# Kernel tuning notes

Measured on AMD Instinct MI355X. Metric: run time of the kernel, lower is better.

The kernel has to match this reference:

```python
import jax, jax.numpy as jnp
import numpy as np

D_LATENTS = 256
B, N = 8, 4096
EPS = 1e-5  # BatchNorm eps (torch default)


def _w(k, shape):
    return jax.random.normal(k, shape, jnp.float32) * 0.05


def setup_inputs() -> dict:
    key = jax.random.key(0)
    ks = jax.random.split(key, 20)
    d4, d2, d = D_LATENTS // 4, D_LATENTS // 2, D_LATENTS
    def bn(k):
        k1, k2 = jax.random.split(k)
        g = 1.0 + 0.1 * jax.random.normal(k1, (0,), jnp.float32)  # placeholder
        return g
    inp = {
        "x": jax.random.normal(ks[0], (B, 3, N), jnp.float32),
        "conv1_w": _w(ks[1], (d4, 3)),
        "bn1_g": 1.0 + 0.1 * jax.random.normal(ks[2], (d4,), jnp.float32),
        "bn1_b": 0.1 * jax.random.normal(ks[3], (d4,), jnp.float32),
        "conv2_w": _w(ks[4], (d4, d4)),
        "bn2_g": 1.0 + 0.1 * jax.random.normal(ks[5], (d4,), jnp.float32),
        "bn2_b": 0.1 * jax.random.normal(ks[6], (d4,), jnp.float32),
        "le0_w1": _w(ks[7], (d2, d2)),
        "le0_g1": 1.0 + 0.1 * jax.random.normal(ks[8], (d2,), jnp.float32),
        "le0_b1": 0.1 * jax.random.normal(ks[9], (d2,), jnp.float32),
        "le0_w2": _w(ks[10], (d2, d2)),
        "le0_g2": 1.0 + 0.1 * jax.random.normal(ks[11], (d2,), jnp.float32),
        "le0_b2": 0.1 * jax.random.normal(ks[12], (d2,), jnp.float32),
        "le1_w1": _w(ks[13], (d, d)),
        "le1_g1": 1.0 + 0.1 * jax.random.normal(ks[14], (d,), jnp.float32),
        "le1_b1": 0.1 * jax.random.normal(ks[15], (d,), jnp.float32),
        "le1_w2": _w(ks[16], (d, d)),
        "le1_g2": 1.0 + 0.1 * jax.random.normal(ks[17], (d,), jnp.float32),
        "le1_b2": 0.1 * jax.random.normal(ks[18], (d,), jnp.float32),
    }
    return inp


def _bn_relu(y, g, b, axes, ch_axis):
    # BatchNorm (training-mode batch stats, biased var like torch) + ReLU
    m = jnp.mean(y, axes, keepdims=True)
    v = jnp.var(y, axes, keepdims=True)
    shp = [1] * y.ndim
    shp[ch_axis] = -1
    return jax.nn.relu((y - m) * jax.lax.rsqrt(v + EPS) * g.reshape(shp) + b.reshape(shp))


def _square_distance(src, dst):
    # src [B,S,3], dst [B,N,3] -> [B,S,N]
    return (jnp.sum(src * src, -1, keepdims=True)
            - 2.0 * jnp.einsum('bsc,bnc->bsn', src, dst)
            + jnp.sum(dst * dst, -1)[:, None, :])


def _fps(xyz, npoint):
    # farthest point sampling, deterministic start at index 0
    Bb, Nn, _ = xyz.shape
    def step(carry, _):
        dist_min, farthest = carry
        centroid = jnp.take_along_axis(xyz, farthest[:, None, None], axis=1)  # [B,1,3]
        d = jnp.sum((xyz - centroid) ** 2, -1)  # [B,N]
        dist_min = jnp.minimum(dist_min, d)
        nxt = jnp.argmax(dist_min, -1).astype(jnp.int32)
        return (dist_min, nxt), farthest
    init = (jnp.full((Bb, Nn), 1e10, xyz.dtype), jnp.zeros((Bb,), jnp.int32))
    _, idxs = jax.lax.scan(step, init, None, length=npoint)
    return jnp.transpose(idxs)  # [B, npoint]


def _sample_and_group(npoint, nsample, xyz, points):
    # PCT-style: FPS centers, kNN neighbors (radius unused), concat(rel, center)
    Bb = xyz.shape[0]
    fps_idx = _fps(xyz, npoint)                       # [B,S]
    bidx = jnp.arange(Bb)[:, None]
    new_xyz = xyz[bidx, fps_idx]                      # [B,S,3]
    new_pts = points[bidx, fps_idx]                   # [B,S,D]
    d2 = _square_distance(new_xyz, xyz)               # [B,S,N]
    _, knn_idx = jax.lax.top_k(-d2, nsample)          # [B,S,ns]
    grouped = points[jnp.arange(Bb)[:, None, None], knn_idx]  # [B,S,ns,D]
    center = new_pts[:, :, None, :]
    feat = jnp.concatenate([grouped - center,
                            jnp.broadcast_to(center, grouped.shape)], axis=-1)
    return new_xyz, feat  # [B,S,3], [B,S,ns,2D]


def _local_encoder(x4, w1, g1, b1, w2, g2, b2):
    # x4: [b,n,s,d] -> conv1x1/bn/relu x2 over channel dim, max over s -> [b,out,n]
    y = jnp.einsum('bnsd,od->bnos', x4, w1)
    y = _bn_relu(y, g1, b1, (0, 1, 3), 2)
    y = jnp.einsum('bnis,oi->bnos', y, w2)
    y = _bn_relu(y, g2, b2, (0, 1, 3), 2)
    y = jnp.max(y, axis=3)                # [b,n,out]
    return jnp.transpose(y, (0, 2, 1))    # [b,out,n]


def reference(x, conv1_w, bn1_g, bn1_b, conv2_w, bn2_g, bn2_b,
              le0_w1, le0_g1, le0_b1, le0_w2, le0_g2, le0_b2,
              le1_w1, le1_g1, le1_b1, le1_w2, le1_g2, le1_b2):
    xyz = jnp.transpose(x, (0, 2, 1))                 # [B,N,3]
    y = jnp.einsum('bcn,oc->bon', x, conv1_w)
    y = _bn_relu(y, bn1_g, bn1_b, (0, 2), 1)
    y = jnp.einsum('bcn,oc->bon', y, conv2_w)
    y = _bn_relu(y, bn2_g, bn2_b, (0, 2), 1)
    pts = jnp.transpose(y, (0, 2, 1))                 # [B,N,d4]
    new_xyz, feat = _sample_and_group(512, 32, xyz, pts)       # [B,512,32,d2]
    f0 = _local_encoder(feat, le0_w1, le0_g1, le0_b1, le0_w2, le0_g2, le0_b2)  # [B,d2,512]
    pts1 = jnp.transpose(f0, (0, 2, 1))
    _, feat2 = _sample_and_group(256, 32, new_xyz, pts1)       # [B,256,32,d]
    f1 = _local_encoder(feat2, le1_w1, le1_g1, le1_b1, le1_w2, le1_g2, le1_b2)  # [B,d,256]
    return f1
```

## Files before the change

### kernel.cpp

```cpp
#include <hip/hip_runtime.h>

constexpr int B_  = 8;
constexpr int N_  = 4096;
constexpr int NP1 = 512;
constexpr int NP2 = 256;
constexpr float EPS_ = 1e-5f;

typedef __attribute__((ext_vector_type(8))) short bhalf8;
typedef __attribute__((ext_vector_type(4))) float f32x4;

__device__ inline short f2bf(float f) {
  union { float fv; unsigned u; } v; v.fv = f;
  unsigned r = v.u + 0x7FFFu + ((v.u >> 16) & 1u);
  return (short)(r >> 16);
}
__device__ inline float bf2f(short s) {
  return __uint_as_float(((unsigned)(unsigned short)s) << 16);
}

template<int CTRL>
__device__ inline void dpp_amax(unsigned &khi, unsigned &klo) {
  unsigned ohi = (unsigned)__builtin_amdgcn_mov_dpp((int)khi, CTRL, 0xF, 0xF, false);
  unsigned olo = (unsigned)__builtin_amdgcn_mov_dpp((int)klo, CTRL, 0xF, 0xF, false);
  if (ohi > khi || (ohi == khi && olo > klo)) { khi = ohi; klo = olo; }
}
__device__ inline void swz16_amax(unsigned &khi, unsigned &klo) {
  unsigned ohi = (unsigned)__builtin_amdgcn_ds_swizzle((int)khi, 0x401F);
  unsigned olo = (unsigned)__builtin_amdgcn_ds_swizzle((int)klo, 0x401F);
  if (ohi > khi || (ohi == khi && olo > klo)) { khi = ohi; klo = olo; }
}
__device__ inline void x32_amax(unsigned &khi, unsigned &klo) {
  unsigned ohi = (unsigned)__shfl_xor((int)khi, 32);
  unsigned olo = (unsigned)__shfl_xor((int)klo, 32);
  if (ohi > khi || (ohi == khi && olo > klo)) { khi = ohi; klo = olo; }
}
__device__ inline unsigned ford(float f) {
  unsigned u = __float_as_uint(f);
  return u ^ (((unsigned)((int)u >> 31)) | 0x80000000u);
}

constexpr int S_BN1 = 0;
constexpr int S_BN2 = 128;
constexpr int S_L0A = 256;
constexpr int S_L0B = 512;
constexpr int S_L1A = 768;
constexpr int S_L1B = 1280;
constexpr int S_TOTAL = 1792;

constexpr size_t OFF_T1   = 0;
constexpr size_t OFF_YBUF = OFF_T1   + 2097152;
constexpr size_t OFF_PTS1 = OFF_YBUF + 16777216;
constexpr size_t OFF_NXYZ = OFF_PTS1 + 524288;
constexpr size_t OFF_WT2C = OFF_NXYZ + 12288;
constexpr size_t OFF_BW0A = OFF_WT2C + 4096;
constexpr size_t OFF_BW0B = OFF_BW0A + 8192;
constexpr size_t OFF_BW1A = OFF_BW0B + 8192;
constexpr size_t OFF_BW1B = OFF_BW1A + 32768;
constexpr size_t OFF_STAT = OFF_BW1B + 32768;
constexpr size_t OFF_CNT  = OFF_STAT + S_TOTAL;
constexpr size_t OFF_INT  = OFF_CNT + 32;

__device__ inline void prep_elem(int idx, const float* __restrict__ conv2w,
                                 const float* __restrict__ w0a, const float* __restrict__ w0b,
                                 const float* __restrict__ w1a, const float* __restrict__ w1b,
                                 float* __restrict__ wt2c,
                                 short* __restrict__ b0a, short* __restrict__ b0b,
                                 short* __restrict__ b1a, short* __restrict__ b1b) {
  if (idx < 4096) { int d = idx >> 6, o = idx & 63; wt2c[idx] = conv2w[o*64 + d]; return; }
  idx -= 4096;
  const float* w; short* dst; int D;
  if      (idx <  2048) { w = w0a; dst = b0a; D = 128; }
  else if (idx <  4096) { w = w0b; dst = b0b; D = 128; idx -= 2048; }
  else if (idx < 12288) { w = w1a; dst = b1a; D = 256; idx -= 4096; }
  else                  { w = w1b; dst = b1b; D = 256; idx -= 12288; }
  int kblk = idx / D, o = idx % D;
  const float* src = w + (size_t)o*D + kblk*8;
  bhalf8 pk;
#pragma unroll
  for (int j = 0; j < 8; ++j) pk[j] = f2bf(src[j]);
  *(bhalf8*)&dst[(size_t)idx*8] = pk;
}

struct FpsSmem {
  float lx[4096], ly[4096], lz[4096];
  float sx[512], sy[512], sz[512];
  unsigned long long wk[2][8];
  int seli1[512];
  int seli2[256];
};
struct ConvSmem {
  float xs[3][64];
  float redS[4][64], redQ[4][64];
  float sc[64], sh[64];
  float at[64*68];
};

__global__ __launch_bounds__(256) void front_kernel(
    const float* __restrict__ x,
    const float* __restrict__ conv1w, const float* __restrict__ bn1g, const float* __restrict__ bn1b,
    const float* __restrict__ conv2w, const float* __restrict__ bn2g, const float* __restrict__ bn2b,
    const float* __restrict__ w0a, const float* __restrict__ w0b,
    const float* __restrict__ w1a, const float* __restrict__ w1b,
    float* __restrict__ wt2c,
    short* __restrict__ b0a, short* __restrict__ b0b,
    short* __restrict__ b1a, short* __restrict__ b1b,
    float* __restrict__ t1, float* __restrict__ t2,
    float* __restrict__ stats, int* __restrict__ cnt,
    int* __restrict__ sel1, float* __restrict__ nxyz, int* __restrict__ sel2) {
  __shared__ __align__(16) char smem_raw[sizeof(FpsSmem)];
  int t = threadIdx.x;
  if (blockIdx.x < 8) {
    constexpr int NPTS = 4096, NSEL1 = 512, NSEL2 = 256, NT = 256;
    constexpr int K = NPTS / NT, NS = NT / 32;
    FpsSmem& S = *reinterpret_cast<FpsSmem*>(smem_raw);
    int b = blockIdx.x;
    int lane = t & 63, wid = t >> 6;
    const float* cb = x + (size_t)b * 3 * NPTS;
    for (int i = t; i < NPTS; i += NT) {
      S.lx[i] = cb[i]; S.ly[i] = cb[NPTS + i]; S.lz[i] = cb[2*NPTS + i];
    }
    __syncthreads();
    float px[K], py[K], pz[K], dm[K];
#pragma unroll
    for (int k = 0; k < K; ++k) {
      int p = t + k*NT;
      px[k] = S.lx[p]; py[k] = S.ly[p]; pz[k] = S.lz[p];
      dm[k] = 1e10f;
    }
    float cx = S.lx[0], cy = S.ly[0], cz = S.lz[0];
    if (t == 0) { S.seli1[0] = 0; S.sx[0] = cx; S.sy[0] = cy; S.sz[0] = cz; }
    for (int it = 1; it < NSEL1; ++it) {
      float bv = -1.f; int bi = 0;
#pragma unroll
      for (int k = 0; k < K; ++k) {
        float dx = px[k]-cx, dy = py[k]-cy, dz = pz[k]-cz;
        float d = dx*dx + dy*dy + dz*dz;
        float nd = fminf(dm[k], d);
        dm[k] = nd;
        if (nd > bv) { bv = nd; bi = t + k*NT; }
      }
      unsigned khi = __float_as_uint(bv), klo = ~(unsigned)bi;
      dpp_amax<0xB1>(khi, klo);
      dpp_amax<0x4E>(khi, klo);
      dpp_amax<0x141>(khi, klo);
      dpp_amax<0x140>(khi, klo);
      swz16_amax(khi, klo);
      int p = it & 1;
      if ((lane & 31) == 0)
        S.wk[p][wid*2 + (lane >> 5)] = ((unsigned long long)khi << 32) | klo;
      __syncthreads();
      unsigned long long best = S.wk[p][0];
#pragma unroll
      for (int i2 = 1; i2 < NS; ++i2) { unsigned long long v2 = S.wk[p][i2]; if (v2 > best) best = v2; }
      int Bi = (int)(~(unsigned)best);
      cx = S.lx[Bi]; cy = S.ly[Bi]; cz = S.lz[Bi];
      if (t == 0) { S.seli1[it] = Bi; S.sx[it] = cx; S.sy[it] = cy; S.sz[it] = cz; }
    }
    __syncthreads();
    if (t < 64) {
      constexpr int K2 = NSEL1 / 64;
      float qx[K2], qy[K2], qz[K2], dm2[K2];
#pragma unroll
      for (int k = 0; k < K2; ++k) {
        int p = t + k*64;
        qx[k] = S.sx[p]; qy[k] = S.sy[p]; qz[k] = S.sz[p];
        dm2[k] = 1e10f;
      }
      cx = S.sx[0]; cy = S.sy[0]; cz = S.sz[0];
      if (t == 0) S.seli2[0] = 0;
      for (int it = 1; it < NSEL2; ++it) {
        float bv = -1.f; int bi = 0;
#pragma unroll
        for (int k = 0; k < K2; ++k) {
          float dx = qx[k]-cx, dy = qy[k]-cy, dz = qz[k]-cz;
          float d = dx*dx + dy*dy + dz*dz;
          float nd = fminf(dm2[k], d);
          dm2[k] = nd;
          if (nd > bv) { bv = nd; bi = t + k*64; }
        }
        unsigned khi = __float_as_uint(bv), klo = ~(unsigned)bi;
        dpp_amax<0xB1>(khi, klo);
        dpp_amax<0x4E>(khi, klo);
        dpp_amax<0x141>(khi, klo);
        dpp_amax<0x140>(khi, klo);
        swz16_amax(khi, klo);
        x32_amax(khi, klo);
        int Bi = (int)~klo;
        cx = S.sx[Bi]; cy = S.sy[Bi]; cz = S.sz[Bi];
        if (t == 0) S.seli2[it] = Bi;
      }
    } else {
      for (int i = t - 64; i < NSEL1; i += NT - 64) {
        sel1[(size_t)b*NSEL1 + i] = S.seli1[i];
        float* q = nxyz + ((size_t)b*NSEL1 + i)*3;
        q[0] = S.sx[i]; q[1] = S.sy[i]; q[2] = S.sz[i];
      }
    }
    __syncthreads();
    for (int i = t; i < NSEL2; i += NT) sel2[(size_t)b*NSEL2 + i] = S.seli2[i];
    return;
  }
  ConvSmem& C = *reinterpret_cast<ConvSmem*>(smem_raw);
  int cb = blockIdx.x - 8;
  { int idx = cb*256 + t;
    if (idx < 24576) prep_elem(idx, conv2w, w0a, w0b, w1a, w1b, wt2c, b0a, b0b, b1a, b1b); }
  for (int tile = cb; tile < 512; tile += 256) {
    int b = tile >> 6, n0 = (tile & 63) << 6;
    if (t < 192) { int c = t >> 6, nl = t & 63; C.xs[c][nl] = x[((size_t)b*3 + c)*N_ + n0 + nl]; }
    __syncthreads();
    int o = t & 63, ng = t >> 6;
    float w0 = conv1w[o*3+0], w1 = conv1w[o*3+1], w2 = conv1w[o*3+2];
    float ls = 0.f, lq = 0.f;
#pragma unroll
    for (int k = 0; k < 16; ++k) {
      int nl = ng*16 + k;
      float y = C.xs[0][nl]*w0 + C.xs[1][nl]*w1 + C.xs[2][nl]*w2;
      t1[((size_t)b*N_ + n0 + nl)*64 + o] = y;
      ls += y; lq += y*y;
    }
    C.redS[ng][o] = ls; C.redQ[ng][o] = lq;
    __syncthreads();
    if (t < 64) {
      float s = C.redS[0][t]+C.redS[1][t]+C.redS[2][t]+C.redS[3][t];
      float q = C.redQ[0][t]+C.redQ[1][t]+C.redQ[2][t]+C.redQ[3][t];
      atomicAdd(&stats[S_BN1 + t], s);
      atomicAdd(&stats[S_BN1 + 64 + t], q);
    }
    __syncthreads();
  }
  if (t == 0) {
    __threadfence();
    __hip_atomic_fetch_add(&cnt[0], 1, __ATOMIC_ACQ_REL, __HIP_MEMORY_SCOPE_AGENT);
    while (__hip_atomic_load(&cnt[0], __ATOMIC_ACQUIRE, __HIP_MEMORY_SCOPE_AGENT) < 256)
      __builtin_amdgcn_s_sleep(8);
    __threadfence();
  }
  __syncthreads();
  if (t < 64) {
    float m = stats[S_BN1 + t] * (1.f/32768.f);
    float v = stats[S_BN1 + 64 + t] * (1.f/32768.f) - m*m;
    float s = bn1g[t] * rsqrtf(v + EPS_);
    C.sc[t] = s; C.sh[t] = bn1b[t] - m*s;
  }
  __syncthreads();
  for (int tile = cb; tile < 512; tile += 256) {
    int b = tile >> 6, n0 = (tile & 63) << 6;
    constexpr int P = 68;
    for (int e = t; e < 4096; e += 256) {
      int nl = e >> 6, c = e & 63;
      float v = t1[((size_t)b*N_ + n0 + nl)*64 + c];
      C.at[c*P + nl] = fmaxf(v*C.sc[c] + C.sh[c], 0.f);
    }
    __syncthreads();
    int o = t & 63, ng = t >> 6;
    float acc[16];
#pragma unroll
    for (int k = 0; k < 16; ++k) acc[k] = 0.f;
    for (int i = 0; i < 64; ++i) {
      float wv = wt2c[i*64 + o];
      const float* ar = &C.at[i*P + ng*16];
#pragma unroll
      for (int k = 0; k < 16; k += 4) {
        float4 a4 = *(const float4*)(ar + k);
        acc[k+0] += a4.x*wv; acc[k+1] += a4.y*wv;
        acc[k+2] += a4.z*wv; acc[k+3] += a4.w*wv;
      }
    }
    float ls = 0.f, lq = 0.f;
#pragma unroll
    for (int k = 0; k < 16; ++k) {
      float y = acc[k];
      t2[((size_t)b*N_ + n0 + ng*16 + k)*64 + o] = y;
      ls += y; lq += y*y;
    }
    C.redS[ng][o] = ls; C.redQ[ng][o] = lq;
    __syncthreads();
    if (t < 64) {
      float s = C.redS[0][t]+C.redS[1][t]+C.redS[2][t]+C.redS[3][t];
      float q = C.redQ[0][t]+C.redQ[1][t]+C.redQ[2][t]+C.redQ[3][t];
      atomicAdd(&stats[S_BN2 + t], s);
      atomicAdd(&stats[S_BN2 + 64 + t], q);
    }
    __syncthreads();
  }
  if (t == 0) {
    __threadfence();
    __hip_atomic_fetch_add(&cnt[1], 1, __ATOMIC_ACQ_REL, __HIP_MEMORY_SCOPE_AGENT);
    while (__hip_atomic_load(&cnt[1], __ATOMIC_ACQUIRE, __HIP_MEMORY_SCOPE_AGENT) < 256)
      __builtin_amdgcn_s_sleep(8);
    __threadfence();
  }
  __syncthreads();
  {
    int o = t & 63;
    float m = stats[S_BN2 + o] * (1.f/32768.f);
    float v = stats[S_BN2 + 64 + o] * (1.f/32768.f) - m*m;
    float s = bn2g[o] * rsqrtf(v + EPS_);
    float sh = bn2b[o] - m*s;
    for (int tile = cb; tile < 512; tile += 256)
#pragma unroll
      for (int j = 0; j < 16; ++j) {
        size_t idx = (size_t)tile*4096 + j*256 + t;
        t1[idx] = fmaxf(t2[idx]*s + sh, 0.f);
      }
  }
}

template<int NDST, bool XLAY>
__device__ inline void wave_knn(const float* __restrict__ db,
                                float qx, float qy, float qz,
                                int* __restrict__ out32) {
  constexpr int K = NDST / 64;
  int lane = threadIdx.x & 63;
  float q2 = (qx*qx + qy*qy) + qz*qz;
  float d2r[K];
#pragma unroll
  for (int k = 0; k < K; ++k) {
    int j = lane + k*64;
    float xx, yy, zz;
    if (XLAY) { xx = db[j]; yy = db[NDST + j]; zz = db[2*NDST + j]; }
    else      { xx = db[j*3]; yy = db[j*3+1]; zz = db[j*3+2]; }
    float dot = (qx*xx + qy*yy) + qz*zz;
    float p2  = (xx*xx + yy*yy) + zz*zz;
    d2r[k] = (q2 - 2.f*dot) + p2;
  }
  int myout = 0;
  for (int r = 0; r < 32; ++r) {
    float bv = 3e38f; int bi = lane;
#pragma unroll
    for (int k = 0; k < K; ++k) {
      float v = d2r[k];
      if (v < bv) { bv = v; bi = lane + k*64; }
    }
    unsigned khi = ~ford(bv), klo = ~(unsigned)bi;
    dpp_amax<0xB1>(khi, klo);
    dpp_amax<0x4E>(khi, klo);
    dpp_amax<0x141>(khi, klo);
    dpp_amax<0x140>(khi, klo);
    swz16_amax(khi, klo);
    x32_amax(khi, klo);
    int Bi = (int)~klo;
    if (lane == r) myout = Bi;
#pragma unroll
    for (int k = 0; k < K; ++k)
      if (lane + k*64 == Bi) d2r[k] = 3e38f;
  }
  if (lane < 32) out32[lane] = myout;
}

__global__ __launch_bounds__(256) void knn_fused_kernel(
    const float* __restrict__ x, const float* __restrict__ nxyz,
    const int* __restrict__ sel2, int* __restrict__ knn1, int* __restrict__ knn2) {
  int wid = threadIdx.x >> 6;
  int blk = blockIdx.x;
  if (blk < 1024) {
    int q = blk*4 + wid;
    int b = q >> 9, qi = q & 511;
    const float* qp = nxyz + ((size_t)b*NP1 + qi)*3;
    wave_knn<4096, true>(x + (size_t)b*3*N_, qp[0], qp[1], qp[2], knn1 + (size_t)q*32);
  } else {
    int q = (blk - 1024)*4 + wid;
    int b = q >> 8, qi = q & 255;
    int qrow = b*NP1 + sel2[b*NP2 + qi];
    const float* qp = nxyz + (size_t)qrow*3;
    wave_knn<512, false>(nxyz + (size_t)b*NP1*3, qp[0], qp[1], qp[2], knn2 + (size_t)q*32);
  }
}

template<int D, int PW, int NP, int SRCN, int SOFF>
__global__ __launch_bounds__(256) void gemm1_kernel(
    const float* __restrict__ pts, const int* __restrict__ knn,
    const int* __restrict__ cent, const short* __restrict__ bw,
    short* __restrict__ ybuf, float* __restrict__ stats) {
  constexpr int KB = D/8;
  __shared__ __align__(16) short As[64*D];
  __shared__ float cen_s[2*PW];
  __shared__ int kid_s[64];
  __shared__ float sstat[2*D];
  int t = threadIdx.x, blk = blockIdx.x;
  int g0 = blk*2;
  if (t < 64) {
    int grp = t >> 5, s = t & 31;
    kid_s[t] = knn[((size_t)(g0+grp))*32 + s];
  }
  for (int i = t; i < 2*PW; i += 256) {
    int grp = i / PW, d = i % PW;
    int g = g0 + grp; int b = g / NP; int ci = cent[g];
    cen_s[i] = pts[((size_t)b*SRCN + ci)*PW + d];
  }
  for (int i = t; i < 2*D; i += 256) sstat[i] = 0.f;
  __syncthreads();
  for (int task = t; task < 64*KB; task += 256) {
    int row = task / KB, c = task % KB;
    int grp = row >> 5;
    int g = g0 + grp; int b = g / NP;
    int d = c*8;
    float v0,v1,v2,v3,v4,v5,v6,v7;
    if (d < PW) {
      const float* src = pts + ((size_t)b*SRCN + kid_s[row])*PW + d;
      float4 x0 = *(const float4*)src, x1 = *(const float4*)(src+4);
      const float* cc = &cen_s[grp*PW + d];
      v0=x0.x-cc[0]; v1=x0.y-cc[1]; v2=x0.z-cc[2]; v3=x0.w-cc[3];
      v4=x1.x-cc[4]; v5=x1.y-cc[5]; v6=x1.z-cc[6]; v7=x1.w-cc[7];
    } else {
      const float* cc = &cen_s[grp*PW + d - PW];
      v0=cc[0]; v1=cc[1]; v2=cc[2]; v3=cc[3]; v4=cc[4]; v5=cc[5]; v6=cc[6]; v7=cc[7];
    }
    bhalf8 pk;
    pk[0]=f2bf(v0); pk[1]=f2bf(v1); pk[2]=f2bf(v2); pk[3]=f2bf(v3);
    pk[4]=f2bf(v4); pk[5]=f2bf(v5); pk[6]=f2bf(v6); pk[7]=f2bf(v7);
    int a16 = row*KB + (c ^ (row & 7));
    *(bhalf8*)&As[a16*8] = pk;
  }
  __syncthreads();
  int w = t >> 6, l = t & 63, lr = l & 15, lg = l >> 4;
  f32x4 acc[D/16];
#pragma unroll
  for (int ct = 0; ct < D/16; ++ct) acc[ct] = (f32x4){0.f,0.f,0.f,0.f};
  int r = w*16 + lr;
#pragma unroll
  for (int kg = 0; kg < D/32; ++kg) {
    int c = (kg*4 + lg) ^ (r & 7);
    bhalf8 af = *(const bhalf8*)&As[(r*KB + c)*8];
#pragma unroll
    for (int ct = 0; ct < D/16; ++ct) {
      bhalf8 bf = *(const bhalf8*)&bw[((size_t)(kg*4 + lg)*D + ct*16 + lr)*8];
      acc[ct] = __builtin_amdgcn_mfma_f32_16x16x32_bf16(af, bf, acc[ct], 0, 0, 0);
    }
  }
  __syncthreads();
  int lrow = w*16 + lg*4;
#pragma unroll
  for (int ct = 0; ct < D/16; ++ct) {
    int col = ct*16 + lr;
    f32x4 a = acc[ct];
    As[(lrow+0)*D + col] = f2bf(a[0]);
    As[(lrow+1)*D + col] = f2bf(a[1]);
    As[(lrow+2)*D + col] = f2bf(a[2]);
    As[(lrow+3)*D + col] = f2bf(a[3]);
    float s = a[0]+a[1]+a[2]+a[3];
    float q = a[0]*a[0]+a[1]*a[1]+a[2]*a[2]+a[3]*a[3];
    s += __shfl_xor(s, 16); q += __shfl_xor(q, 16);
    s += __shfl_xor(s, 32); q += __shfl_xor(q, 32);
    if (lg == 0) { atomicAdd(&sstat[col], s); atomicAdd(&sstat[D+col], q); }
  }
  __syncthreads();
  {
    short* yp = ybuf + (size_t)blk*64*D;
    for (int i = t; i < 64*D/8; i += 256)
      *(bhalf8*)&yp[i*8] = *(const bhalf8*)&As[i*8];
  }
  for (int i = t; i < 2*D; i += 256) atomicAdd(&stats[SOFF+i], sstat[i]);
}

template<int D, int SIN, int SOUT, int CNT>
__global__ __launch_bounds__(256) void gemm2_kernel(
    const float* __restrict__ g1, const float* __restrict__ b1,
    const short* __restrict__ bw, const short* __restrict__ ybuf,
    float* __restrict__ mm, float* __restrict__ stats) {
  __shared__ __align__(16) float scsh[2*D];
  __shared__ float sstat[2*D];
  __shared__ float wmax[4][D], wmin[4][D];
  int t = threadIdx.x, blk = blockIdx.x;
  for (int i = t; i < D; i += 256) {
    float m = stats[SIN + i] * (1.f/(float)CNT);
    float v = stats[SIN + D + i] * (1.f/(float)CNT) - m*m;
    float s = g1[i] * rsqrtf(v + EPS_);
    scsh[i] = s; scsh[D+i] = b1[i] - m*s;
  }
  for (int i = t; i < 2*D; i += 256) sstat[i] = 0.f;
  __syncthreads();
  int w = t >> 6, l = t & 63, lr = l & 15, lg = l >> 4;
  size_t row = (size_t)blk*64 + w*16 + lr;
  const short* yrow = ybuf + row*D;
  f32x4 acc[D/16];
#pragma unroll
  for (int ct = 0; ct < D/16; ++ct) acc[ct] = (f32x4){0.f,0.f,0.f,0.f};
#pragma unroll
  for (int kg = 0; kg < D/32; ++kg) {
    int k = kg*32 + lg*8;
    bhalf8 yv = *(const bhalf8*)(yrow + k);
    bhalf8 af;
#pragma unroll
    for (int j = 0; j < 8; ++j)
      af[j] = f2bf(fmaxf(bf2f(yv[j])*scsh[k+j] + scsh[D+k+j], 0.f));
#pragma unroll
    for (int ct = 0; ct < D/16; ++ct) {
      bhalf8 bf = *(const bhalf8*)&bw[((size_t)(kg*4 + lg)*D + ct*16 + lr)*8];
      acc[ct] = __builtin_amdgcn_mfma_f32_16x16x32_bf16(af, bf, acc[ct], 0, 0, 0);
    }
  }
#pragma unroll
  for (int ct = 0; ct < D/16; ++ct) {
    int col = ct*16 + lr;
    f32x4 a = acc[ct];
    float mx = fmaxf(fmaxf(a[0], a[1]), fmaxf(a[2], a[3]));
    float mn = fminf(fminf(a[0], a[1]), fminf(a[2], a[3]));
    mx = fmaxf(mx, __shfl_xor(mx, 16)); mn = fminf(mn, __shfl_xor(mn, 16));
    mx = fmaxf(mx, __shfl_xor(mx, 32)); mn = fminf(mn, __shfl_xor(mn, 32));
    if (lg == 0) { wmax[w][col] = mx; wmin[w][col] = mn; }
    float s = a[0]+a[1]+a[2]+a[3];
    float q = a[0]*a[0]+a[1]*a[1]+a[2]*a[2]+a[3]*a[3];
    s += __shfl_xor(s, 16); q += __shfl_xor(q, 16);
    s += __shfl_xor(s, 32); q += __shfl_xor(q, 32);
    if (lg == 0) { atomicAdd(&sstat[col], s); atomicAdd(&sstat[D+col], q); }
  }
  __syncthreads();
  for (int i = t; i < 2*D; i += 256) {
    int g = i / D, col = i - g*D;
    float mx = fmaxf(wmax[2*g][col], wmax[2*g+1][col]);
    float mn = fminf(wmin[2*g][col], wmin[2*g+1][col]);
    float* mp = mm + ((size_t)blk*2 + g)*2*D;
    mp[col] = mx; mp[D + col] = mn;
    atomicAdd(&stats[SOUT+i], sstat[i]);
  }
}

template<int D, int NP, int SOFF, int CNT, bool TR>
__global__ __launch_bounds__(256) void le3_kernel(
    const float* __restrict__ g2, const float* __restrict__ b2,
    const float* __restrict__ mm, const float* __restrict__ stats,
    float* __restrict__ out) {
  int idx = blockIdx.x*256 + threadIdx.x;
  int g = idx / D, o = idx - g*D;
  float m = stats[SOFF + o] * (1.f/(float)CNT);
  float v = stats[SOFF + D + o] * (1.f/(float)CNT) - m*m;
  float s = g2[o] * rsqrtf(v + EPS_);
  float sh = b2[o] - m*s;
  const float* mp = mm + (size_t)g*2*D;
  float pick = (s >= 0.f) ? mp[o] : mp[D + o];
  float r = fmaxf(pick*s + sh, 0.f);
  if (TR) { int b = g / NP, n = g - b*NP; out[((size_t)b*D + o)*NP + n] = r; }
  else    out[(size_t)g*D + o] = r;
}

extern "C" void kernel_launch(void* const* d_in, const int* in_sizes, int n_in,
                              void* d_out, int out_size, void* d_ws, size_t ws_size,
                              hipStream_t stream) {
  (void)in_sizes; (void)n_in; (void)out_size; (void)ws_size;
  const float* x       = (const float*)d_in[0];
  const float* conv1_w = (const float*)d_in[1];
  const float* bn1_g   = (const float*)d_in[2];
  const float* bn1_b   = (const float*)d_in[3];
  const float* conv2_w = (const float*)d_in[4];
  const float* bn2_g   = (const float*)d_in[5];
  const float* bn2_b   = (const float*)d_in[6];
  const float* le0_w1  = (const float*)d_in[7];
  const float* le0_g1  = (const float*)d_in[8];
  const float* le0_b1  = (const float*)d_in[9];
  const float* le0_w2  = (const float*)d_in[10];
  const float* le0_g2  = (const float*)d_in[11];
  const float* le0_b2  = (const float*)d_in[12];
  const float* le1_w1  = (const float*)d_in[13];
  const float* le1_g1  = (const float*)d_in[14];
  const float* le1_b1  = (const float*)d_in[15];
  const float* le1_w2  = (const float*)d_in[16];
  const float* le1_g2  = (const float*)d_in[17];
  const float* le1_b2  = (const float*)d_in[18];

  float* ws   = (float*)d_ws;
  float* t1   = ws + OFF_T1;
  float* t2   = ws + OFF_YBUF;
  short* ybuf = (short*)(ws + OFF_YBUF);
  float* mm   = t1;
  float* pts1 = ws + OFF_PTS1;
  float* nxyz = ws + OFF_NXYZ;
  float* wt2c = ws + OFF_WT2C;
  short* bw0a = (short*)(ws + OFF_BW0A);
  short* bw0b = (short*)(ws + OFF_BW0B);
  short* bw1a = (short*)(ws + OFF_BW1A);
  short* bw1b = (short*)(ws + OFF_BW1B);
  float* stats = ws + OFF_STAT;
  int*   cnt   = (int*)(ws + OFF_CNT);
  int* fps1 = (int*)(ws + OFF_INT);
  int* fps2 = fps1 + 4096;
  int* knn1 = fps2 + 2048;
  int* knn2 = knn1 + 131072;

  hipMemsetAsync(stats, 0, (S_TOTAL + 32)*sizeof(float), stream);
  front_kernel<<<264, 256, 0, stream>>>(x,
      conv1_w, bn1_g, bn1_b, conv2_w, bn2_g, bn2_b,
      le0_w1, le0_w2, le1_w1, le1_w2,
      wt2c, bw0a, bw0b, bw1a, bw1b,
      t1, t2, stats, cnt, fps1, nxyz, fps2);

  knn_fused_kernel<<<1536, 256, 0, stream>>>(x, nxyz, fps2, knn1, knn2);

  gemm1_kernel<128,  64, 512, 4096, S_L0A><<<2048, 256, 0, stream>>>(t1, knn1, fps1, bw0a, ybuf, stats);
  gemm2_kernel<128, S_L0A, S_L0B, 131072><<<2048, 256, 0, stream>>>(le0_g1, le0_b1, bw0b, ybuf, mm, stats);
  le3_kernel<128, 512, S_L0B, 131072, false><<<2048, 256, 0, stream>>>(le0_g2, le0_b2, mm, stats, pts1);

  gemm1_kernel<256, 128, 256,  512, S_L1A><<<1024, 256, 0, stream>>>(pts1, knn2, fps2, bw1a, ybuf, stats);
  gemm2_kernel<256, S_L1A, S_L1B, 65536><<<1024, 256, 0, stream>>>(le1_g1, le1_b1, bw1b, ybuf, mm, stats);
  le3_kernel<256, 256, S_L1B, 65536, true><<<2048, 256, 0, stream>>>(le1_g2, le1_b2, mm, stats, (float*)d_out);
}
```

Measured before the change: 924.9 us.

## Fuse kNN search into gemm1 kernels and drop separate kNN launch

Removes the standalone kNN kernel. Each gemm1 block now runs the kNN query for its two groups, using two of its four waves, and writes the neighbour indices straight into shared memory. This drops a launch and the global write and read of the knn index buffers. In exchange, two waves sit idle at the barrier during the search, and the search now runs at gemm1's occupancy, which its shared-memory use limits.

Result: slower. 1.039 ms (+12.3%).

```diff
diff --git a/kernel.cpp b/kernel.cpp
--- a/kernel.cpp
+++ b/kernel.cpp
@@ -348,29 +348,12 @@
   if (lane < 32) out32[lane] = myout;
 }
 
-__global__ __launch_bounds__(256) void knn_fused_kernel(
-    const float* __restrict__ x, const float* __restrict__ nxyz,
-    const int* __restrict__ sel2, int* __restrict__ knn1, int* __restrict__ knn2) {
-  int wid = threadIdx.x >> 6;
-  int blk = blockIdx.x;
-  if (blk < 1024) {
-    int q = blk*4 + wid;
-    int b = q >> 9, qi = q & 511;
-    const float* qp = nxyz + ((size_t)b*NP1 + qi)*3;
-    wave_knn<4096, true>(x + (size_t)b*3*N_, qp[0], qp[1], qp[2], knn1 + (size_t)q*32);
-  } else {
-    int q = (blk - 1024)*4 + wid;
-    int b = q >> 8, qi = q & 255;
-    int qrow = b*NP1 + sel2[b*NP2 + qi];
-    const float* qp = nxyz + (size_t)qrow*3;
-    wave_knn<512, false>(nxyz + (size_t)b*NP1*3, qp[0], qp[1], qp[2], knn2 + (size_t)q*32);
-  }
-}
-
-template<int D, int PW, int NP, int SRCN, int SOFF>
+template<int D, int PW, int NP, int SRCN, int SOFF, int NDST, bool XLAY>
 __global__ __launch_bounds__(256) void gemm1_kernel(
-    const float* __restrict__ pts, const int* __restrict__ knn,
-    const int* __restrict__ cent, const short* __restrict__ bw,
+    const float* __restrict__ qdb,
+    const float* __restrict__ pts,
+    const int* __restrict__ cent, const int* __restrict__ qmap,
+    const float* __restrict__ nxyz, const short* __restrict__ bw,
     short* __restrict__ ybuf, float* __restrict__ stats) {
   constexpr int KB = D/8;
   __shared__ __align__(16) short As[64*D];
@@ -379,9 +362,16 @@
   __shared__ float sstat[2*D];
   int t = threadIdx.x, blk = blockIdx.x;
   int g0 = blk*2;
-  if (t < 64) {
-    int grp = t >> 5, s = t & 31;
-    kid_s[t] = knn[((size_t)(g0+grp))*32 + s];
+  {
+    int wid = t >> 6;
+    if (wid < 2) {
+      int g = g0 + wid;
+      int b = g / NP, qi = g - b*NP;
+      int qrow = b*NP1 + (qmap ? qmap[g] : qi);
+      const float* qp = nxyz + (size_t)qrow*3;
+      const float* db = XLAY ? (qdb + (size_t)b*3*SRCN) : (nxyz + (size_t)b*NP1*3);
+      wave_knn<NDST, XLAY>(db, qp[0], qp[1], qp[2], &kid_s[wid*32]);
+    }
   }
   for (int i = t; i < 2*PW; i += 256) {
     int grp = i / PW, d = i % PW;
@@ -574,8 +564,6 @@
   int*   cnt   = (int*)(ws + OFF_CNT);
   int* fps1 = (int*)(ws + OFF_INT);
   int* fps2 = fps1 + 4096;
-  int* knn1 = fps2 + 2048;
-  int* knn2 = knn1 + 131072;
 
   hipMemsetAsync(stats, 0, (S_TOTAL + 32)*sizeof(float), stream);
   front_kernel<<<264, 256, 0, stream>>>(x,
@@ -584,13 +572,13 @@
       wt2c, bw0a, bw0b, bw1a, bw1b,
       t1, t2, stats, cnt, fps1, nxyz, fps2);
 
-  knn_fused_kernel<<<1536, 256, 0, stream>>>(x, nxyz, fps2, knn1, knn2);
-
-  gemm1_kernel<128,  64, 512, 4096, S_L0A><<<2048, 256, 0, stream>>>(t1, knn1, fps1, bw0a, ybuf, stats);
+  gemm1_kernel<128,  64, 512, 4096, S_L0A, 4096, true ><<<2048, 256, 0, stream>>>(
+      x, t1, fps1, nullptr, nxyz, bw0a, ybuf, stats);
   gemm2_kernel<128, S_L0A, S_L0B, 131072><<<2048, 256, 0, stream>>>(le0_g1, le0_b1, bw0b, ybuf, mm, stats);
   le3_kernel<128, 512, S_L0B, 131072, false><<<2048, 256, 0, stream>>>(le0_g2, le0_b2, mm, stats, pts1);
 
-  gemm1_kernel<256, 128, 256,  512, S_L1A><<<1024, 256, 0, stream>>>(pts1, knn2, fps2, bw1a, ybuf, stats);
+  gemm1_kernel<256, 128, 256,  512, S_L1A,  512, false><<<1024, 256, 0, stream>>>(
+      nxyz, pts1, fps2, fps2, nxyz, bw1a, ybuf, stats);
   gemm2_kernel<256, S_L1A, S_L1B, 65536><<<1024, 256, 0, stream>>>(le1_g1, le1_b1, bw1b, ybuf, mm, stats);
   le3_kernel<256, 256, S_L1B, 65536, true><<<2048, 256, 0, stream>>>(le1_g2, le1_b2, mm, stats, (float*)d_out);
 }
```
